# Kernel tuning notes

Hardware: AMD Instinct MI355X
Metric: run time of the kernel (lower is better)

The kernel has to match this reference:

```python
import jax, jax.numpy as jnp
import numpy as np
import math

CH = 512
HEADS = 8
GROUPS = 32
EPS = 1e-5


def group_norm(x, w, b):
    # x: [B, C, T]
    B, C, T = x.shape
    xg = x.reshape(B, GROUPS, C // GROUPS, T)
    mu = xg.mean(axis=(2, 3), keepdims=True)
    var = xg.var(axis=(2, 3), keepdims=True)
    xg = (xg - mu) * jax.lax.rsqrt(var + EPS)
    return xg.reshape(B, C, T) * w[None, :, None] + b[None, :, None]


def conv1x1(x, w, b):
    # x: [B, C, T], w: [O, C, 1]
    return jnp.einsum('oc,bct->bot', w[:, :, 0], x) + b[None, :, None]


def conv3_same(x, w, b):
    y = jax.lax.conv_general_dilated(x, w, window_strides=(1,), padding='SAME',
                                     dimension_numbers=('NCH', 'OIH', 'NCH'))
    return y + b[None, :, None]


def setup_inputs() -> dict:
    key = jax.random.key(0)
    ks = jax.random.split(key, 12)
    B, Ti, Ts = 2, 4096, 1024
    inp = {
        'image': jax.random.normal(ks[0], (B, Ti, CH), jnp.float32),
        'st': jax.random.normal(ks[1], (B, Ts, CH), jnp.float32),
        'xn_w': jnp.ones((CH,), jnp.float32),
        'xn_b': jnp.zeros((CH,), jnp.float32),
        'jn_w': jnp.ones((CH,), jnp.float32),
        'jn_b': jnp.zeros((CH,), jnp.float32),
        'xqkv_w': jax.random.normal(ks[2], (3 * CH, CH, 1), jnp.float32) * (1.0 / math.sqrt(CH)),
        'xqkv_b': jnp.zeros((3 * CH,), jnp.float32),
        'jqkv_w': jax.random.normal(ks[3], (3 * CH, CH, 1), jnp.float32) * (1.0 / math.sqrt(CH)),
        'jqkv_b': jnp.zeros((3 * CH,), jnp.float32),
        # NOTE: original zero-inits proj; we use small random weights so the
        # attention path contributes to the output (same math).
        'proj_w': jax.random.normal(ks[4], (CH, CH, 3), jnp.float32) * (0.02 / math.sqrt(3 * CH)),
        'proj_b': jnp.zeros((CH,), jnp.float32),
    }
    return inp


def reference(image, st, xn_w, xn_b, jn_w, jn_b, xqkv_w, xqkv_b, jqkv_w, jqkv_b, proj_w, proj_b):
    # image: [B, Ti, C]  st: [B, Ts, C]
    x = image.transpose(0, 2, 1)           # [B, C, Ti]
    jc = st.transpose(0, 2, 1)              # [B, C, Ts]

    x_qkv = conv1x1(group_norm(x, xn_w, xn_b), xqkv_w, xqkv_b)    # [B, 3C, Ti]
    jc_qkv = conv1x1(group_norm(jc, jn_w, jn_b), jqkv_w, jqkv_b)  # [B, 3C, Ts]

    B, _, Ti = x_qkv.shape
    ch = CH // HEADS
    scale = 1.0 / math.sqrt(math.sqrt(ch))

    img_q = x_qkv[:, :CH].reshape(B, HEADS, ch, Ti)
    st_k = jc_qkv[:, CH:2 * CH].reshape(B, HEADS, ch, -1)
    st_v = jc_qkv[:, 2 * CH:].reshape(B, HEADS, ch, -1)

    # cross-attention: image queries attend to st keys/values
    w = jnp.einsum('bhct,bhcs->bhts', img_q * scale, st_k * scale)  # [B,H,Ti,Ts]
    w = jax.nn.softmax(w.astype(jnp.float32), axis=-1).astype(w.dtype)
    attn = jnp.einsum('bhts,bhcs->bhct', w, st_v).reshape(B, CH, Ti)

    x_h = conv3_same(attn, proj_w, proj_b)
    return x + x_h  # [B, C, Ti]
```

## Files before the change

kernel.cpp:

```cpp
#include <hip/hip_runtime.h>
#include <math.h>

static constexpr int CH = 512;
static constexpr int GROUPS = 32;
static constexpr int HC = 64;
static constexpr float EPS = 1e-5f;
static constexpr int TI = 4096;
static constexpr int TS = 1024;

typedef __bf16 bf16x8 __attribute__((ext_vector_type(8)));
typedef __bf16 bf16x4 __attribute__((ext_vector_type(4)));
typedef float f32x4 __attribute__((ext_vector_type(4)));

__global__ __launch_bounds__(256) void k_gn_partial(const float* __restrict__ img,
                                                    const float* __restrict__ st,
                                                    double* __restrict__ part) {
  int bi = blockIdx.x;
  int which = bi >> 9;
  int rem = bi & 511;
  int b = rem >> 8;
  int g = (rem >> 3) & 31;
  int chunk = rem & 7;
  const float* X = which ? st : img;
  int T = which ? TS : TI;
  int rows = T >> 3;
  int tid = threadIdx.x;
  const float* base = X + ((size_t)b * T + (size_t)chunk * rows) * CH + g * 16;
  double s1 = 0.0, s2 = 0.0;
  for (int t = tid; t < rows; t += 256) {
    const float4* p = (const float4*)(base + (size_t)t * CH);
#pragma unroll
    for (int q = 0; q < 4; ++q) {
      float4 v = p[q];
      s1 += (double)v.x + (double)v.y + (double)v.z + (double)v.w;
      s2 += (double)v.x * v.x + (double)v.y * v.y + (double)v.z * v.z + (double)v.w * v.w;
    }
  }
  __shared__ double r1[256];
  __shared__ double r2[256];
  r1[tid] = s1;
  r2[tid] = s2;
  __syncthreads();
  for (int s = 128; s > 0; s >>= 1) {
    if (tid < s) { r1[tid] += r1[tid + s]; r2[tid] += r2[tid + s]; }
    __syncthreads();
  }
  if (tid == 0) {
    part[bi * 2 + 0] = r1[0];
    part[bi * 2 + 1] = r2[0];
  }
}

__global__ __launch_bounds__(128) void k_gn_final(const double* __restrict__ part,
                                                  float* __restrict__ stats_x,
                                                  float* __restrict__ stats_j) {
  int tid = threadIdx.x;
  int which = tid >> 6;
  int idx = tid & 63;
  const double* p = part + ((which << 9) + ((idx >> 5) << 8) + ((idx & 31) << 3)) * 2;
  double s1 = 0.0, s2 = 0.0;
#pragma unroll
  for (int c = 0; c < 8; ++c) {
    s1 += p[c * 2 + 0];
    s2 += p[c * 2 + 1];
  }
  int T = which ? TS : TI;
  double N = 16.0 * T;
  double mu = s1 / N;
  double var = s2 / N - mu * mu;
  float rs = (float)(1.0 / sqrt(var + (double)EPS));
  float* stats = which ? stats_j : stats_x;
  stats[idx * 2 + 0] = (float)mu;
  stats[idx * 2 + 1] = rs;
}

__global__ __launch_bounds__(256) void k_gn_apply2(const float* __restrict__ img,
                                                   const float* __restrict__ st,
                                                   const float* __restrict__ stats_x,
                                                   const float* __restrict__ stats_j,
                                                   const float* __restrict__ xn_w,
                                                   const float* __restrict__ xn_b,
                                                   const float* __restrict__ jn_w,
                                                   const float* __restrict__ jn_b,
                                                   __bf16* __restrict__ Xnp,
                                                   __bf16* __restrict__ stnp) {
  int bi = blockIdx.x;
  bool isimg = bi < 2048;
  const float* X = isimg ? img : st;
  const float* stats = isimg ? stats_x : stats_j;
  const float* nw = isimg ? xn_w : jn_w;
  const float* nb = isimg ? xn_b : jn_b;
  __bf16* Xp = isimg ? Xnp : stnp;
  int T = isimg ? TI : TS;
  size_t idx = ((size_t)(isimg ? bi : bi - 2048) * 256 + threadIdx.x) * 8;

  int b = (int)(idx / ((size_t)T * 512));
  size_t rem = idx - (size_t)b * T * 512;
  int t = (int)(rem >> 9);
  int c = (int)(rem & 511);
  int g = c >> 4;
  float mu = stats[(b * GROUPS + g) * 2 + 0];
  float rs = stats[(b * GROUPS + g) * 2 + 1];
  float4 v0 = *(const float4*)(X + idx);
  float4 v1 = *(const float4*)(X + idx + 4);
  float4 w0 = *(const float4*)(nw + c);
  float4 w1 = *(const float4*)(nw + c + 4);
  float4 q0 = *(const float4*)(nb + c);
  float4 q1 = *(const float4*)(nb + c + 4);
  float xv[8] = {v0.x, v0.y, v0.z, v0.w, v1.x, v1.y, v1.z, v1.w};
  float wv[8] = {w0.x, w0.y, w0.z, w0.w, w1.x, w1.y, w1.z, w1.w};
  float qv[8] = {q0.x, q0.y, q0.z, q0.w, q1.x, q1.y, q1.z, q1.w};
  bf16x8 r;
#pragma unroll
  for (int i = 0; i < 8; ++i) {
    float a = rs * wv[i];
    r[i] = (__bf16)fmaf(xv[i], a, qv[i] - mu * a);
  }
  size_t off = ((((size_t)b * (T >> 4) + (t >> 4)) * 16 + (c >> 5)) * 64 +
                ((c >> 3) & 3) * 16 + (t & 15)) * 8;
  *(bf16x8*)(Xp + off) = r;
}

__global__ __launch_bounds__(256) void k_pack_all(const float* __restrict__ xqkv_w,
                                                  const float* __restrict__ jqkv_w,
                                                  const float* __restrict__ proj_w,
                                                  __bf16* __restrict__ wqb,
                                                  __bf16* __restrict__ wkvb,
                                                  __bf16* __restrict__ wb3) {
  int bi = blockIdx.x;
  if (bi < 384) {
    const float* W = (bi < 128) ? xqkv_w : (jqkv_w + (size_t)CH * CH);
    __bf16* Wp = (bi < 128) ? wqb : wkvb;
    int idx = ((bi < 128) ? bi : bi - 128) * 256 + threadIdx.x;
    int lane = idx & 63;
    int l = lane & 15, g = lane >> 4;
    int cb = (idx >> 6) & 15;
    int ob = idx >> 10;
    const float* src = W + (size_t)(ob * 16 + l) * 512 + cb * 32 + g * 8;
    float4 v0 = *(const float4*)src;
    float4 v1 = *(const float4*)(src + 4);
    float xv[8] = {v0.x, v0.y, v0.z, v0.w, v1.x, v1.y, v1.z, v1.w};
    bf16x8 r;
#pragma unroll
    for (int i = 0; i < 8; ++i) r[i] = (__bf16)xv[i];
    *(bf16x8*)(Wp + (size_t)idx * 8) = r;
  } else {
    int idx = (bi - 384) * 256 + threadIdx.x;
    int lane = idx & 63;
    int l = lane & 15, g = lane >> 4;
    int ob = (idx >> 6) & 31;
    int q = idx >> 11;
    int tap = q % 3;
    int cb = q / 3;
    int o = ob * 16 + l;
    int c = cb * 32 + g * 8;
    bf16x8 r;
#pragma unroll
    for (int j = 0; j < 8; ++j) r[j] = (__bf16)proj_w[((size_t)o * 512 + c + j) * 3 + tap];
    *(bf16x8*)(wb3 + (size_t)idx * 8) = r;
  }
}

__global__ __launch_bounds__(256) void k_qkv_mfma(const __bf16* __restrict__ Xp,
                                                  const __bf16* __restrict__ Wp,
                                                  const float* __restrict__ bias,
                                                  __bf16* __restrict__ outQK,
                                                  __bf16* __restrict__ outVp,
                                                  int T) {
  int b = blockIdx.z;
  int o0 = blockIdx.y * 64;
  int tid = threadIdx.x;
  int w = tid >> 6;
  int lane = tid & 63;
  int l = lane & 15;
  int g = lane >> 4;
  int t0 = blockIdx.x * 128 + w * 32;
  int Tb = T >> 4;
  bool vmode = (outVp != nullptr) && (o0 >= 512);

  __shared__ __align__(16) __bf16 Elds[4][2048];

  f32x4 acc[2][4] = {};
  const __bf16* Xb = Xp + (size_t)b * T * 512;

  auto load_c = [&](int cb, bf16x8 (&af)[2], bf16x8 (&wf)[4]) {
#pragma unroll
    for (int m = 0; m < 2; ++m)
      af[m] = *(const bf16x8*)(Xb + ((((size_t)(t0 >> 4) + m) * 16 + cb) * 64 + lane) * 8);
#pragma unroll
    for (int n = 0; n < 4; ++n)
      wf[n] = *(const bf16x8*)(Wp + ((((size_t)(o0 >> 4) + n) * 16 + cb) * 64 + lane) * 8);
  };

  bf16x8 afA[2], wfA[4], afB[2], wfB[4];
#define QKV_LOOP(MMEXPR)                                                        \
  {                                                                             \
    load_c(0, afA, wfA);                                                        \
    _Pragma("unroll") for (int cb = 0; cb < 16; cb += 2) {                      \
      load_c(cb + 1, afB, wfB);                                                 \
      _Pragma("unroll") for (int m = 0; m < 2; ++m)                             \
          _Pragma("unroll") for (int n = 0; n < 4; ++n) {                       \
        bf16x8 af = afA[m], wf = wfA[n];                                        \
        acc[m][n] = MMEXPR;                                                     \
      }                                                                         \
      if (cb + 2 < 16) load_c(cb + 2, afA, wfA);                                \
      _Pragma("unroll") for (int m = 0; m < 2; ++m)                             \
          _Pragma("unroll") for (int n = 0; n < 4; ++n) {                       \
        bf16x8 af = afB[m], wf = wfB[n];                                        \
        acc[m][n] = MMEXPR;                                                     \
      }                                                                         \
    }                                                                           \
  }

  if (!vmode) {
    QKV_LOOP(__builtin_amdgcn_mfma_f32_16x16x32_bf16(wf, af, acc[m][n], 0, 0, 0))
    float sc = (outVp == nullptr) ? 0.125f * 1.44269504088896f : 1.0f;
    int swz = (l & 7) << 1;
    __bf16(*Eq)[64] = reinterpret_cast<__bf16(*)[64]>(&Elds[w][0]);
#pragma unroll
    for (int m = 0; m < 2; ++m)
#pragma unroll
      for (int n = 0; n < 4; ++n) {
        f32x4 bv = *(const f32x4*)(bias + o0 + 16 * n + 4 * g);
        bf16x4 pv;
#pragma unroll
        for (int r = 0; r < 4; ++r) pv[r] = (__bf16)((acc[m][n][r] + bv[r]) * sc);
        *(bf16x4*)&Eq[m * 16 + l][((4 * n + g) ^ swz) * 4] = pv;
      }
#pragma unroll
    for (int m = 0; m < 2; ++m)
#pragma unroll
      for (int cbi = 0; cbi < 2; ++cbi) {
        bf16x8 v = *(const bf16x8*)&Eq[m * 16 + l][((8 * cbi + 2 * g) ^ swz) * 4];
        *(bf16x8*)(outQK +
                   ((((size_t)b * Tb + (t0 >> 4) + m) * 16 + (o0 >> 5) + cbi) * 64 + lane) * 8) = v;
      }
  } else {
    QKV_LOOP(__builtin_amdgcn_mfma_f32_16x16x32_bf16(af, wf, acc[m][n], 0, 0, 0))
    int swzv = l & 6;
    __bf16(*Ev)[32] = reinterpret_cast<__bf16(*)[32]>(&Elds[w][0]);
#pragma unroll
    for (int m = 0; m < 2; ++m)
#pragma unroll
      for (int n = 0; n < 4; ++n) {
        float bo = bias[o0 + 16 * n + l];
        bf16x4 pv;
#pragma unroll
        for (int r = 0; r < 4; ++r) pv[r] = (__bf16)(acc[m][n][r] + bo);
        *(bf16x4*)&Ev[16 * n + l][((4 * m + g) ^ swzv) * 4] = pv;
      }
#pragma unroll
    for (int n = 0; n < 4; ++n) {
      bf16x8 v = *(const bf16x8*)&Ev[16 * n + l][((2 * g) ^ swzv) * 4];
      int cb16 = ((o0 - 512) >> 4) + n;
      *(bf16x8*)(outVp + ((((size_t)b * 32 + cb16) * 32 + (t0 >> 5)) * 64 + lane) * 8) = v;
    }
  }
#undef QKV_LOOP
}

__global__ __launch_bounds__(128, 4) void k_attn_mfma(const __bf16* __restrict__ Qp,
                                                      const __bf16* __restrict__ Kp,
                                                      const __bf16* __restrict__ Vp,
                                                      __bf16* __restrict__ outA) {
  int b = blockIdx.z;
  int h = blockIdx.y;
  int tid = threadIdx.x;
  int w = tid >> 6;
  int lane = tid & 63;
  int l = lane & 15;
  int g = lane >> 4;
  int t0 = blockIdx.x * 32;
  int swz = (l & 7) << 1;

  __shared__ __align__(16) __bf16 Pt[2][2][16][64];
  __shared__ float Lred[64][2];
  float* Ored = (float*)&Pt[0][0][0][0];

  bf16x8 qf[2][2];
#pragma unroll
  for (int m = 0; m < 2; ++m)
#pragma unroll
    for (int ks = 0; ks < 2; ++ks)
      qf[m][ks] = *(const bf16x8*)(Qp + ((((size_t)b * 256 + (t0 >> 4) + m) * 16 +
                                          2 * h + ks) * 64 + lane) * 8);

  f32x4 o_acc[2][4] = {};
  float rs_acc[2] = {};

  int s_base = w * 512;
#pragma unroll 1
  for (int s0 = s_base; s0 < s_base + 512; s0 += 64) {
    bf16x8 kf[4][2];
#pragma unroll
    for (int n = 0; n < 4; ++n)
#pragma unroll
      for (int ks = 0; ks < 2; ++ks)
        kf[n][ks] = *(const bf16x8*)(Kp + ((((size_t)b * 64 + (s0 >> 4) + n) * 16 +
                                            2 * h + ks) * 64 + lane) * 8);
    bf16x8 vf[4][2];
#pragma unroll
    for (int n = 0; n < 4; ++n)
#pragma unroll
      for (int ks = 0; ks < 2; ++ks)
        vf[n][ks] = *(const bf16x8*)(Vp + ((((size_t)b * 32 + h * 4 + n) * 32 +
                                            (s0 >> 5) + ks) * 64 + lane) * 8);
    f32x4 sT[4][2];
#pragma unroll
    for (int sb = 0; sb < 4; ++sb)
#pragma unroll
      for (int tb = 0; tb < 2; ++tb) {
        f32x4 z = {0.f, 0.f, 0.f, 0.f};
        z = __builtin_amdgcn_mfma_f32_16x16x32_bf16(kf[sb][0], qf[tb][0], z, 0, 0, 0);
        sT[sb][tb] = __builtin_amdgcn_mfma_f32_16x16x32_bf16(kf[sb][1], qf[tb][1], z, 0, 0, 0);
      }
#pragma unroll
    for (int tb = 0; tb < 2; ++tb)
#pragma unroll
      for (int sb = 0; sb < 4; ++sb) {
        float p0 = exp2f(sT[sb][tb][0]);
        float p1 = exp2f(sT[sb][tb][1]);
        float p2 = exp2f(sT[sb][tb][2]);
        float p3 = exp2f(sT[sb][tb][3]);
        rs_acc[tb] += (p0 + p1) + (p2 + p3);
        bf16x4 pv;
        pv[0] = (__bf16)p0;
        pv[1] = (__bf16)p1;
        pv[2] = (__bf16)p2;
        pv[3] = (__bf16)p3;
        *(bf16x4*)&Pt[w][tb][l][((4 * sb + g) ^ swz) * 4] = pv;
      }
    bf16x8 pa[2][2];
#pragma unroll
    for (int tb = 0; tb < 2; ++tb)
#pragma unroll
      for (int ks = 0; ks < 2; ++ks)
        pa[tb][ks] = *(const bf16x8*)&Pt[w][tb][l][((8 * ks + 2 * g) ^ swz) * 4];
#pragma unroll
    for (int tb = 0; tb < 2; ++tb)
#pragma unroll
      for (int n = 0; n < 4; ++n) {
        o_acc[tb][n] = __builtin_amdgcn_mfma_f32_16x16x32_bf16(vf[n][0], pa[tb][0], o_acc[tb][n], 0, 0, 0);
        o_acc[tb][n] = __builtin_amdgcn_mfma_f32_16x16x32_bf16(vf[n][1], pa[tb][1], o_acc[tb][n], 0, 0, 0);
      }
  }

  __syncthreads();
  if (w == 1) {
#pragma unroll
    for (int tb = 0; tb < 2; ++tb) {
#pragma unroll
      for (int n = 0; n < 4; ++n)
#pragma unroll
        for (int r = 0; r < 4; ++r) Ored[lane * 32 + tb * 16 + n * 4 + r] = o_acc[tb][n][r];
      Lred[lane][tb] = rs_acc[tb];
    }
  }
  __syncthreads();
  if (w == 0) {
#pragma unroll
    for (int tb = 0; tb < 2; ++tb) {
#pragma unroll
      for (int n = 0; n < 4; ++n)
#pragma unroll
        for (int r = 0; r < 4; ++r) o_acc[tb][n][r] += Ored[lane * 32 + tb * 16 + n * 4 + r];
      float v = rs_acc[tb] + Lred[lane][tb];
      v += __shfl_xor(v, 16, 64);
      v += __shfl_xor(v, 32, 64);
      float inv = 1.f / v;
#pragma unroll
      for (int n = 0; n < 4; ++n) {
        bf16x4 ov;
#pragma unroll
        for (int r = 0; r < 4; ++r) ov[r] = (__bf16)(o_acc[tb][n][r] * inv);
        *(bf16x4*)(outA + ((size_t)b * TI + t0 + 16 * tb + l) * 512 + h * 64 + 16 * n + 4 * g) = ov;
      }
    }
  }
}

__global__ __launch_bounds__(256) void k_conv3_mfma(const __bf16* __restrict__ A,
                                                    const __bf16* __restrict__ W3p,
                                                    const float* __restrict__ bias,
                                                    const float* __restrict__ image,
                                                    float* __restrict__ out) {
  int b = blockIdx.z;
  int o0 = blockIdx.y * 64;
  int ob0 = o0 >> 4;
  int tid = threadIdx.x;
  int w = tid >> 6;
  int lane = tid & 63;
  int l = lane & 15;
  int g = lane >> 4;
  int t0 = blockIdx.x * 128;
  int t0w = t0 + w * 32;

  __shared__ __align__(16) __bf16 Alds[2][130 * 32];
  __shared__ __align__(16) __bf16 Wlds[2][12 * 512];

  const __bf16* Ab = A + (size_t)b * TI * 512;

  auto stage = [&](int cb, int buf) {
#pragma unroll
    for (int pass = 0; pass < 3; ++pass) {
      int gi = tid + pass * 256;
      if (gi < 520) {
        int r = gi >> 2, gg = gi & 3;
        int t = t0 - 1 + r;
        bf16x8 v = {};
        if (t >= 0 && t < TI) v = *(const bf16x8*)(Ab + (size_t)t * 512 + cb * 32 + gg * 8);
        *(bf16x8*)&Alds[buf][r * 32 + ((gg ^ (r & 3)) << 3)] = v;
      }
    }
#pragma unroll
    for (int ch = w; ch < 12; ch += 4) {
      bf16x8 v = *(const bf16x8*)(W3p + ((((size_t)cb * 3 + (ch >> 2)) * 32 + ob0 +
                                          (ch & 3)) * 64 + lane) * 8);
      *(bf16x8*)&Wlds[buf][ch * 512 + lane * 8] = v;
    }
  };

  f32x4 acc[2][4] = {};

  stage(0, 0);
  __syncthreads();
#pragma unroll 1
  for (int cs = 0; cs < 16; ++cs) {
    int cur = cs & 1;
    if (cs < 15) stage(cs + 1, cur ^ 1);
    bf16x8 af[3][2], wf[3][4];
#pragma unroll
    for (int tap = 0; tap < 3; ++tap) {
#pragma unroll
      for (int m = 0; m < 2; ++m) {
        int r = w * 32 + 16 * m + l + tap;
        af[tap][m] = *(const bf16x8*)&Alds[cur][r * 32 + ((g ^ (r & 3)) << 3)];
      }
#pragma unroll
      for (int n = 0; n < 4; ++n)
        wf[tap][n] = *(const bf16x8*)&Wlds[cur][(tap * 4 + n) * 512 + lane * 8];
    }
#pragma unroll
    for (int tap = 0; tap < 3; ++tap)
#pragma unroll
      for (int m = 0; m < 2; ++m)
#pragma unroll
        for (int n = 0; n < 4; ++n)
          acc[m][n] =
              __builtin_amdgcn_mfma_f32_16x16x32_bf16(af[tap][m], wf[tap][n], acc[m][n], 0, 0, 0);
    __syncthreads();
  }

#pragma unroll
  for (int m = 0; m < 2; ++m) {
    int tb = t0w + 16 * m + 4 * g;
#pragma unroll
    for (int n = 0; n < 4; ++n) {
      int o = o0 + 16 * n + l;
      float bo = bias[o];
      f32x4 r;
#pragma unroll
      for (int rr = 0; rr < 4; ++rr)
        r[rr] = acc[m][n][rr] + bo + image[((size_t)b * TI + tb + rr) * CH + o];
      *(f32x4*)(out + ((size_t)b * CH + o) * TI + tb) = r;
    }
  }
}

extern "C" void kernel_launch(void* const* d_in, const int* in_sizes, int n_in,
                              void* d_out, int out_size, void* d_ws, size_t ws_size,
                              hipStream_t stream) {
  const float* image = (const float*)d_in[0];
  const float* st = (const float*)d_in[1];
  const float* xn_w = (const float*)d_in[2];
  const float* xn_b = (const float*)d_in[3];
  const float* jn_w = (const float*)d_in[4];
  const float* jn_b = (const float*)d_in[5];
  const float* xqkv_w = (const float*)d_in[6];
  const float* xqkv_b = (const float*)d_in[7];
  const float* jqkv_w = (const float*)d_in[8];
  const float* jqkv_b = (const float*)d_in[9];
  const float* proj_w = (const float*)d_in[10];
  const float* proj_b = (const float*)d_in[11];
  float* out = (float*)d_out;
  float* ws = (float*)d_ws;

  double* part = (double*)ws;
  float* stats_x = ws + 4096;
  float* stats_j = ws + 4096 + 128;
  __bf16* Xnp = (__bf16*)(ws + 4096 + 256);
  __bf16* abuf = Xnp;
  __bf16* stnp = Xnp + (size_t)2 * TI * CH;
  __bf16* wqb = stnp + (size_t)2 * TS * CH;
  __bf16* wkvb = wqb + (size_t)CH * CH;
  __bf16* wb3 = wkvb + (size_t)2 * CH * CH;
  __bf16* Qp = wb3 + (size_t)3 * CH * CH;
  __bf16* Kp = Qp + (size_t)2 * TI * CH;
  __bf16* Vp = Kp + (size_t)2 * TS * CH;

  k_gn_partial<<<dim3(1024), dim3(256), 0, stream>>>(image, st, part);
  k_gn_final<<<dim3(1), dim3(128), 0, stream>>>(part, stats_x, stats_j);

  k_gn_apply2<<<dim3(2560), dim3(256), 0, stream>>>(image, st, stats_x, stats_j,
                                                    xn_w, xn_b, jn_w, jn_b, Xnp, stnp);

  k_pack_all<<<dim3(768), dim3(256), 0, stream>>>(xqkv_w, jqkv_w, proj_w, wqb, wkvb, wb3);

  k_qkv_mfma<<<dim3(TI / 128, CH / 64, 2), dim3(256), 0, stream>>>(
      Xnp, wqb, xqkv_b, Qp, nullptr, TI);
  k_qkv_mfma<<<dim3(TS / 128, 1024 / 64, 2), dim3(256), 0, stream>>>(
      stnp, wkvb, jqkv_b + CH, Kp, Vp, TS);

  k_attn_mfma<<<dim3(TI / 32, 8, 2), dim3(128), 0, stream>>>(Qp, Kp, Vp, abuf);

  k_conv3_mfma<<<dim3(TI / 128, CH / 64, 2), dim3(256), 0, stream>>>(
      abuf, wb3, proj_b, image, out);
}
```

Baseline: 116.1 us.

## Split attention key range across four waves with tree reduction

The attention kernel now runs four waves per block instead of two, and each wave handles a quarter of the 1024 keys (256) instead of half. The partial output accumulators and row sums are combined through shared memory in a two-level tree reduction. This is meant to shorten each wave's serial key loop and raise the number of waves in flight for latency hiding. In exchange it adds reduction passes with extra __syncthreads, uses more shared memory, and tightens the launch bounds to 256 threads at 8 blocks, which may pressure registers.

```diff
diff --git a/kernel.cpp b/kernel.cpp
--- a/kernel.cpp
+++ b/kernel.cpp
@@ -259,7 +259,7 @@
 #undef QKV_LOOP
 }
 
-__global__ __launch_bounds__(128, 4) void k_attn_mfma(const __bf16* __restrict__ Qp,
+__global__ __launch_bounds__(256, 8) void k_attn_mfma(const __bf16* __restrict__ Qp,
                                                       const __bf16* __restrict__ Kp,
                                                       const __bf16* __restrict__ Vp,
                                                       __bf16* __restrict__ outA) {
@@ -273,9 +273,10 @@
   int t0 = blockIdx.x * 32;
   int swz = (l & 7) << 1;
 
-  __shared__ __align__(16) __bf16 Pt[2][2][16][64];
-  __shared__ float Lred[64][2];
-  float* Ored = (float*)&Pt[0][0][0][0];
+  __shared__ __align__(16) __bf16 Pt[4][2][16][64];
+  __shared__ float LredA[2][64][2];
+  __shared__ float LredB[64][2];
+  float* OredF = (float*)&Pt[0][0][0][0];
 
   bf16x8 qf[2][2];
 #pragma unroll
@@ -288,9 +289,9 @@
   f32x4 o_acc[2][4] = {};
   float rs_acc[2] = {};
 
-  int s_base = w * 512;
+  int s_base = w * 256;
 #pragma unroll 1
-  for (int s0 = s_base; s0 < s_base + 512; s0 += 64) {
+  for (int s0 = s_base; s0 < s_base + 256; s0 += 64) {
     bf16x8 kf[4][2];
 #pragma unroll
     for (int n = 0; n < 4; ++n)
@@ -346,14 +347,38 @@
   }
 
   __syncthreads();
-  if (w == 1) {
+  if (w & 1) {
+    int off = (w >> 1) * 2048 + lane * 32;
 #pragma unroll
     for (int tb = 0; tb < 2; ++tb) {
 #pragma unroll
       for (int n = 0; n < 4; ++n)
 #pragma unroll
-        for (int r = 0; r < 4; ++r) Ored[lane * 32 + tb * 16 + n * 4 + r] = o_acc[tb][n][r];
-      Lred[lane][tb] = rs_acc[tb];
+        for (int r = 0; r < 4; ++r) OredF[off + tb * 16 + n * 4 + r] = o_acc[tb][n][r];
+      LredA[w >> 1][lane][tb] = rs_acc[tb];
+    }
+  }
+  __syncthreads();
+  if (!(w & 1)) {
+    int off = (w >> 1) * 2048 + lane * 32;
+#pragma unroll
+    for (int tb = 0; tb < 2; ++tb) {
+#pragma unroll
+      for (int n = 0; n < 4; ++n)
+#pragma unroll
+        for (int r = 0; r < 4; ++r) o_acc[tb][n][r] += OredF[off + tb * 16 + n * 4 + r];
+      rs_acc[tb] += LredA[w >> 1][lane][tb];
+    }
+  }
+  __syncthreads();
+  if (w == 2) {
+#pragma unroll
+    for (int tb = 0; tb < 2; ++tb) {
+#pragma unroll
+      for (int n = 0; n < 4; ++n)
+#pragma unroll
+        for (int r = 0; r < 4; ++r) OredF[lane * 32 + tb * 16 + n * 4 + r] = o_acc[tb][n][r];
+      LredB[lane][tb] = rs_acc[tb];
     }
   }
   __syncthreads();
@@ -363,8 +388,8 @@
 #pragma unroll
       for (int n = 0; n < 4; ++n)
 #pragma unroll
-        for (int r = 0; r < 4; ++r) o_acc[tb][n][r] += Ored[lane * 32 + tb * 16 + n * 4 + r];
-      float v = rs_acc[tb] + Lred[lane][tb];
+        for (int r = 0; r < 4; ++r) o_acc[tb][n][r] += OredF[lane * 32 + tb * 16 + n * 4 + r];
+      float v = rs_acc[tb] + LredB[lane][tb];
       v += __shfl_xor(v, 16, 64);
       v += __shfl_xor(v, 32, 64);
       float inv = 1.f / v;
@@ -511,7 +536,7 @@
   k_qkv_mfma<<<dim3(TS / 128, 1024 / 64, 2), dim3(256), 0, stream>>>(
       stnp, wkvb, jqkv_b + CH, Kp, Vp, TS);
 
-  k_attn_mfma<<<dim3(TI / 32, 8, 2), dim3(128), 0, stream>>>(Qp, Kp, Vp, abuf);
+  k_attn_mfma<<<dim3(TI / 32, 8, 2), dim3(256), 0, stream>>>(Qp, Kp, Vp, abuf);
 
   k_conv3_mfma<<<dim3(TI / 128, CH / 64, 2), dim3(256), 0, stream>>>(
       abuf, wb3, proj_b, image, out);
```

Measured after the change: 321.3 us. +176.7%, slower.
